# Optimization experiments

Measured on AMD Instinct MI355X. Metric: run time of the kernel, lower is better.

Reference implementation:

```python
import jax, jax.numpy as jnp
import numpy as np

D_IN = 1024
D_OUT = 1024
N, S = 4, 2048

def setup_inputs() -> dict:
    key = jax.random.key(0)
    kv, kk, kq, k1, k2, k3 = jax.random.split(key, 6)
    return {
        "v": jax.random.normal(kv, (N, S, D_IN), dtype=jnp.float32),
        "k": jax.random.normal(kk, (N, S, D_IN), dtype=jnp.float32),
        "q": jax.random.normal(kq, (N, S, D_IN), dtype=jnp.float32),
        "WV": jax.random.normal(k1, (D_OUT, D_IN), dtype=jnp.float32),
        "WQ": jax.random.normal(k2, (D_OUT, D_IN), dtype=jnp.float32),
        "WK": jax.random.normal(k3, (D_OUT, D_IN), dtype=jnp.float32),
    }

def reference(v, k, q, WV, WQ, WK) -> jnp.ndarray:
    # projections: x @ W.T  -> [N, S, D_OUT]
    wv = jnp.einsum('nsw,ow->nso', v, WV)
    wk = jnp.einsum('nsw,ow->nso', k, WK)
    wq = jnp.einsum('nsw,ow->nso', q, WQ)
    # scores [N, Sq, Sk]; NOTE: softmax over axis=1 (query axis, matching torch dim=1),
    # then post-hoc division by input_shape[0] AFTER softmax (faithful to source).
    scores = jnp.einsum('nqo,nko->nqk', wq, wk)
    wqk = jax.nn.softmax(scores, axis=1) / jnp.float32(D_IN)
    return jnp.einsum('nqk,nko->nqo', wqk, wv)
```

## Files before the change

kernel.cpp:

```cpp
#include <hip/hip_runtime.h>
#include <math.h>


typedef _Float16 f16;
typedef _Float16 f16x8 __attribute__((ext_vector_type(8)));
typedef _Float16 f16x4 __attribute__((ext_vector_type(4)));
typedef float f32x4 __attribute__((ext_vector_type(4)));

enum StageMode { SM_PLANES2, SM_PLANES1 };
enum EpiMode   { EPI_F32, EPI_SPLIT, EPI_F16T };

#define GLL_PITCH 32

__device__ __forceinline__ void gll16(const f16* g, f16* l) {
    __builtin_amdgcn_global_load_lds(
        (const __attribute__((address_space(1))) void*)g,
        (__attribute__((address_space(3))) void*)l, 16, 0, 0);
}

__device__ __forceinline__ void stage_gll_plane(const f16* __restrict__ gplane,
                                                f16* __restrict__ lds,
                                                long rowBase, int ld, int k0,
                                                int wave, int lane)
{
#pragma unroll
    for (int i = 0; i < 2; i++) {
        int slotBase = (wave * 2 + i) * 64;
        int t = slotBase + lane;
        int r = t >> 2;
        int c = (t & 3) ^ ((r >> 1) & 3);
        const f16* g = gplane + (rowBase + r) * (long)ld + k0 + c * 8;
        gll16(g, lds + (long)slotBase * 8);
    }
}

__device__ __forceinline__ int frag_off_gll(int row, int g) {
    return row * GLL_PITCH + ((g ^ ((row >> 1) & 3)) << 3);
}

template<StageMode SA, StageMode SB, EpiMode EP, int GROUPM, bool STATS>
__global__ __launch_bounds__(256, 4)
void mfma_gemm(const f16* __restrict__ Ahi, const f16* __restrict__ Alo,
               const f16* __restrict__ Bhi, const f16* __restrict__ Blo,
               float* __restrict__ pmOut, float* __restrict__ psOut,
               void* __restrict__ C0, void* __restrict__ C1,
               int M, int Nc, int K, int lda, int ldb, int ldc,
               long batchA, long batchB, long batchC,
               float epiScale, int tsShift)
{
    constexpr bool TRIPLE = (SA == SM_PLANES2);
    constexpr int PLANE_SZ = 128 * GLL_PITCH;

    int bx, by;
    if constexpr (GROUPM > 0) {
        int gx = gridDim.x;
        int lin = blockIdx.y * gx + blockIdx.x;
        int nig = GROUPM * gx;
        int gid = lin / nig;
        int rem = lin - gid * nig;
        by = gid * GROUPM + (rem % GROUPM);
        bx = rem / GROUPM;
    } else {
        bx = blockIdx.x;
        by = blockIdx.y;
    }
    const int n0 = bx * 128;
    const int m0 = by * 128;
    const long z = blockIdx.z;

    const long aOfs = z * batchA, bOfs = z * batchB, cOfs = z * batchC;

    __shared__ __align__(16) f16 As_hi[PLANE_SZ];
    __shared__ __align__(16) f16 Bs_hi[PLANE_SZ];
    __shared__ __align__(16) f16 As_lo[TRIPLE ? PLANE_SZ : 8];
    __shared__ __align__(16) f16 Bs_lo[TRIPLE ? PLANE_SZ : 8];

    const int tid  = threadIdx.x;
    const int lane = tid & 63;
    const int wave = tid >> 6;
    const int wr = (wave >> 1) * 64;
    const int wc = (wave & 1) * 64;
    const int fm = lane & 15;
    const int fg = lane >> 4;

    f32x4 acc[4][4];
#pragma unroll
    for (int i = 0; i < 4; i++)
#pragma unroll
        for (int j = 0; j < 4; j++) acc[i][j] = (f32x4){0.f, 0.f, 0.f, 0.f};

    int roA[4], roB[4];
#pragma unroll
    for (int i = 0; i < 4; i++) {
        roA[i] = frag_off_gll(wr + i * 16 + fm, fg);
        roB[i] = frag_off_gll(wc + i * 16 + fm, fg);
    }

    for (int k0 = 0; k0 < K; k0 += 32) {
        stage_gll_plane(Ahi + aOfs, As_hi, m0, lda, k0, wave, lane);
        stage_gll_plane(Bhi + bOfs, Bs_hi, n0, ldb, k0, wave, lane);
        if constexpr (TRIPLE) {
            stage_gll_plane(Alo + aOfs, As_lo, m0, lda, k0, wave, lane);
            stage_gll_plane(Blo + bOfs, Bs_lo, n0, ldb, k0, wave, lane);
        }
        __syncthreads();

        f16x8 ah[4], bh[4], al[4], bl[4];
#pragma unroll
        for (int i = 0; i < 4; i++) {
            ah[i] = *(const f16x8*)&As_hi[roA[i]];
            bh[i] = *(const f16x8*)&Bs_hi[roB[i]];
            if constexpr (TRIPLE) {
                al[i] = *(const f16x8*)&As_lo[roA[i]];
                bl[i] = *(const f16x8*)&Bs_lo[roB[i]];
            }
        }
#pragma unroll
        for (int i = 0; i < 4; i++) {
#pragma unroll
            for (int j = 0; j < 4; j++) {
                acc[i][j] = __builtin_amdgcn_mfma_f32_16x16x32_f16(ah[i], bh[j], acc[i][j], 0, 0, 0);
                if constexpr (TRIPLE) {
                    acc[i][j] = __builtin_amdgcn_mfma_f32_16x16x32_f16(ah[i], bl[j], acc[i][j], 0, 0, 0);
                    acc[i][j] = __builtin_amdgcn_mfma_f32_16x16x32_f16(al[i], bh[j], acc[i][j], 0, 0, 0);
                }
            }
        }
        __syncthreads();
    }

    const int cr = fg * 4;
    const int cn = fm;
#pragma unroll
    for (int i = 0; i < 4; i++) {
#pragma unroll
        for (int j = 0; j < 4; j++) {
#pragma unroll
            for (int r = 0; r < 4; r++) {
                long mg = m0 + wr + i * 16 + cr + r;
                long ng = n0 + wc + j * 16 + cn;
                float val = acc[i][j][r] * epiScale;
                if constexpr (EP == EPI_F32) {
                    ((float*)C0)[cOfs + mg * ldc + ng] = val;
                } else if constexpr (EP == EPI_SPLIT) {
                    f16 h = (f16)val;
                    ((f16*)C0)[cOfs + mg * ldc + ng] = h;
                    ((f16*)C1)[cOfs + mg * ldc + ng] = (f16)(val - (float)h);
                } else {
                    long TS = 1L << tsShift;
                    long nb = mg >> tsShift;
                    long s  = mg & (TS - 1);
                    long addr = nb * ((long)Nc << tsShift) + ng * TS + s;
                    ((f16*)C0)[addr] = (f16)val;
                }
            }
        }
    }

    if constexpr (STATS) {
        __shared__ float stM[2][128];
        __shared__ float stS[2][128];
#pragma unroll
        for (int j = 0; j < 4; j++) {
            float mj = -3.402823466e38f;
#pragma unroll
            for (int i = 0; i < 4; i++)
#pragma unroll
                for (int r = 0; r < 4; r++) mj = fmaxf(mj, acc[i][j][r]);
            float sj = 0.f;
#pragma unroll
            for (int i = 0; i < 4; i++)
#pragma unroll
                for (int r = 0; r < 4; r++) sj += __expf(acc[i][j][r] - mj);
#pragma unroll
            for (int mask = 16; mask <= 32; mask <<= 1) {
                float mo = __shfl_xor(mj, mask, 64);
                float so = __shfl_xor(sj, mask, 64);
                float mn = fmaxf(mj, mo);
                sj = sj * __expf(mj - mn) + so * __expf(mo - mn);
                mj = mn;
            }
            if (fg == 0) {
                stM[wave >> 1][wc + j * 16 + cn] = mj;
                stS[wave >> 1][wc + j * 16 + cn] = sj;
            }
        }
        __syncthreads();
        if (tid < 128) {
            float ma = stM[0][tid], mb = stM[1][tid];
            float Mc = fmaxf(ma, mb);
            float Sv = stS[0][tid] * __expf(ma - Mc) + stS[1][tid] * __expf(mb - Mc);
            long o = ((long)z * (M >> 7) + by) * (long)Nc + (long)bx * 128 + tid;
            pmOut[o] = Mc;
            psOut[o] = Sv;
        }
    }
}

__global__ __launch_bounds__(512, 2)
void scores_gemm(const f16* __restrict__ Ahi, const f16* __restrict__ Alo,
                 const f16* __restrict__ Bhi, const f16* __restrict__ Blo,
                 float* __restrict__ pmOut, float* __restrict__ psOut,
                 float* __restrict__ C,
                 int M, int Nc, int K, int lda, int ldb, int ldc,
                 long batchA, long batchB, long batchC)
{
    constexpr int PLANE = 256 * GLL_PITCH;

    __shared__ __align__(16) f16 As_hi[2][PLANE];
    __shared__ __align__(16) f16 As_lo[2][PLANE];
    __shared__ __align__(16) f16 Bs_hi[2][PLANE];
    __shared__ __align__(16) f16 Bs_lo[2][PLANE];

    const int tid  = threadIdx.x;
    const int lane = tid & 63;
    const int wave = tid >> 6;
    const int rw   = wave >> 2;
    const int cw   = wave & 3;
    const int wrM  = rw * 128;
    const int wrN  = cw * 64;
    const int fm   = lane & 15;
    const int fg   = lane >> 4;

    const int Lid = (int)(blockIdx.z * 64 + blockIdx.y * 8 + blockIdx.x);
    const int xcd = Lid & 7;
    const int sct = Lid >> 3;
    const int bxn = sct & 7;
    const int idxp = xcd * 4 + (sct >> 3);
    const int byn = idxp & 7;
    const int zn  = idxp >> 3;

    const int n0 = bxn * 256;
    const int m0 = byn * 256;
    const long z = zn;
    const long aOfs = z * batchA, bOfs = z * batchB, cOfs = z * batchC;

    int slotBase[2], srcA[2], srcB[2];
#pragma unroll
    for (int i = 0; i < 2; i++) {
        int sb = (wave * 2 + i) * 64;
        int t  = sb + lane;
        int r  = t >> 2;
        int c  = (t & 3) ^ ((r >> 1) & 3);
        slotBase[i] = sb * 8;
        srcA[i] = (m0 + r) * lda + c * 8;
        srcB[i] = (n0 + r) * ldb + c * 8;
    }

#define SC_STAGE(buf, k0) do {                                              \
    _Pragma("unroll")                                                        \
    for (int s_ = 0; s_ < 2; s_++) {                                         \
        gll16(Ahi + aOfs + srcA[s_] + (k0), &As_hi[buf][slotBase[s_]]);      \
        gll16(Alo + aOfs + srcA[s_] + (k0), &As_lo[buf][slotBase[s_]]);      \
        gll16(Bhi + bOfs + srcB[s_] + (k0), &Bs_hi[buf][slotBase[s_]]);      \
        gll16(Blo + bOfs + srcB[s_] + (k0), &Bs_lo[buf][slotBase[s_]]);      \
    } } while (0)

    f32x4 acc[8][4];
#pragma unroll
    for (int i = 0; i < 8; i++)
#pragma unroll
        for (int j = 0; j < 4; j++) acc[i][j] = (f32x4){0.f, 0.f, 0.f, 0.f};

    int roA[8], roB[4];
#pragma unroll
    for (int i = 0; i < 8; i++) roA[i] = frag_off_gll(wrM + i * 16 + fm, fg);
#pragma unroll
    for (int j = 0; j < 4; j++) roB[j] = frag_off_gll(wrN + j * 16 + fm, fg);

    const int NT = K >> 5;
    SC_STAGE(0, 0);
    SC_STAGE(1, 32);

    for (int t = 0; t < NT; t++) {
        const int cur = t & 1;
        if (t < NT - 1) {
            asm volatile("s_waitcnt vmcnt(8)" ::: "memory");
        } else {
            asm volatile("s_waitcnt vmcnt(0)" ::: "memory");
        }
        __builtin_amdgcn_sched_barrier(0);
        __builtin_amdgcn_s_barrier();
        __builtin_amdgcn_sched_barrier(0);

        f16x8 bh[4], a0h[4];
#pragma unroll
        for (int j = 0; j < 4; j++) bh[j] = *(const f16x8*)&Bs_hi[cur][roB[j]];
#pragma unroll
        for (int i = 0; i < 4; i++) a0h[i] = *(const f16x8*)&As_hi[cur][roA[i]];
        __builtin_amdgcn_sched_barrier(0);
        f16x8 bl[4], a0l[4];
#pragma unroll
        for (int j = 0; j < 4; j++) bl[j] = *(const f16x8*)&Bs_lo[cur][roB[j]];
#pragma unroll
        for (int i = 0; i < 4; i++) a0l[i] = *(const f16x8*)&As_lo[cur][roA[i]];
        __builtin_amdgcn_sched_barrier(0);

        __builtin_amdgcn_s_setprio(1);
#pragma unroll
        for (int i = 0; i < 4; i++)
#pragma unroll
            for (int j = 0; j < 4; j++)
                acc[i][j] = __builtin_amdgcn_mfma_f32_16x16x32_f16(a0h[i], bh[j], acc[i][j], 0, 0, 0);
        __builtin_amdgcn_s_setprio(0);
        __builtin_amdgcn_sched_barrier(0);

        f16x8 a1h[4], a1l[4];
#pragma unroll
        for (int i = 0; i < 4; i++) {
            a1h[i] = *(const f16x8*)&As_hi[cur][roA[4 + i]];
            a1l[i] = *(const f16x8*)&As_lo[cur][roA[4 + i]];
        }
        __builtin_amdgcn_sched_barrier(0);

        __builtin_amdgcn_s_setprio(1);
#pragma unroll
        for (int i = 0; i < 4; i++)
#pragma unroll
            for (int j = 0; j < 4; j++)
                acc[i][j] = __builtin_amdgcn_mfma_f32_16x16x32_f16(a0h[i], bl[j], acc[i][j], 0, 0, 0);
#pragma unroll
        for (int i = 0; i < 4; i++)
#pragma unroll
            for (int j = 0; j < 4; j++)
                acc[i][j] = __builtin_amdgcn_mfma_f32_16x16x32_f16(a0l[i], bh[j], acc[i][j], 0, 0, 0);
        __builtin_amdgcn_s_setprio(0);

        asm volatile("s_waitcnt lgkmcnt(0)" ::: "memory");
        __builtin_amdgcn_sched_barrier(0);
        __builtin_amdgcn_s_barrier();
        __builtin_amdgcn_sched_barrier(0);

        if (t + 2 < NT) SC_STAGE(cur, (t + 2) * 32);

        __builtin_amdgcn_s_setprio(1);
#pragma unroll
        for (int i = 0; i < 4; i++)
#pragma unroll
            for (int j = 0; j < 4; j++)
                acc[4 + i][j] = __builtin_amdgcn_mfma_f32_16x16x32_f16(a1h[i], bh[j], acc[4 + i][j], 0, 0, 0);
#pragma unroll
        for (int i = 0; i < 4; i++)
#pragma unroll
            for (int j = 0; j < 4; j++)
                acc[4 + i][j] = __builtin_amdgcn_mfma_f32_16x16x32_f16(a1h[i], bl[j], acc[4 + i][j], 0, 0, 0);
#pragma unroll
        for (int i = 0; i < 4; i++)
#pragma unroll
            for (int j = 0; j < 4; j++)
                acc[4 + i][j] = __builtin_amdgcn_mfma_f32_16x16x32_f16(a1l[i], bh[j], acc[4 + i][j], 0, 0, 0);
        __builtin_amdgcn_s_setprio(0);
    }
#undef SC_STAGE

    const int cr = fg * 4;
#pragma unroll
    for (int i = 0; i < 8; i++) {
#pragma unroll
        for (int j = 0; j < 4; j++) {
#pragma unroll
            for (int r = 0; r < 4; r++) {
                long mg = m0 + wrM + i * 16 + cr + r;
                long ng = n0 + wrN + j * 16 + fm;
                C[cOfs + mg * (long)ldc + ng] = acc[i][j][r];
            }
        }
    }

    __shared__ float stM[2][256];
    __shared__ float stS[2][256];
#pragma unroll
    for (int j = 0; j < 4; j++) {
        float mj = -3.402823466e38f;
#pragma unroll
        for (int i = 0; i < 8; i++)
#pragma unroll
            for (int r = 0; r < 4; r++) mj = fmaxf(mj, acc[i][j][r]);
        float sj = 0.f;
#pragma unroll
        for (int i = 0; i < 8; i++)
#pragma unroll
            for (int r = 0; r < 4; r++) sj += __expf(acc[i][j][r] - mj);
#pragma unroll
        for (int mask = 16; mask <= 32; mask <<= 1) {
            float mo = __shfl_xor(mj, mask, 64);
            float so = __shfl_xor(sj, mask, 64);
            float mn = fmaxf(mj, mo);
            sj = sj * __expf(mj - mn) + so * __expf(mo - mn);
            mj = mn;
        }
        if (fg == 0) {
            stM[rw][wrN + j * 16 + fm] = mj;
            stS[rw][wrN + j * 16 + fm] = sj;
        }
    }
    __syncthreads();
    if (tid < 256) {
        float ma = stM[0][tid], mb = stM[1][tid];
        float Mc = fmaxf(ma, mb);
        float Sv = stS[0][tid] * __expf(ma - Mc) + stS[1][tid] * __expf(mb - Mc);
        long o = ((long)z * (M >> 8) + byn) * (long)Nc + (long)bxn * 256 + tid;
        pmOut[o] = Mc;
        psOut[o] = Sv;
    }
}

template<bool HAS_LO>
__global__ __launch_bounds__(256)
void split_kernel(const float* __restrict__ src, f16* __restrict__ hi,
                  f16* __restrict__ lo, long n)
{
    long i = ((long)blockIdx.x * 256 + threadIdx.x) * 8;
    if (i >= n) return;
    float4 x0 = *(const float4*)&src[i];
    float4 x1 = *(const float4*)&src[i + 4];
    float xs[8] = {x0.x, x0.y, x0.z, x0.w, x1.x, x1.y, x1.z, x1.w};
    f16x8 h, l;
#pragma unroll
    for (int e = 0; e < 8; e++) {
        f16 hh = (f16)xs[e];
        h[e] = hh;
        if (HAS_LO) l[e] = (f16)(xs[e] - (float)hh);
    }
    *(f16x8*)&hi[i] = h;
    if (HAS_LO) *(f16x8*)&lo[i] = l;
}

template<int CH>
__global__ __launch_bounds__(64)
void stats_combine_kernel(const float* __restrict__ pm, const float* __restrict__ ps,
                          float* __restrict__ statM, float* __restrict__ statR, int S)
{
    const int n = blockIdx.y;
    const int kk = blockIdx.x * 64 + threadIdx.x;
    float M = -INFINITY;
#pragma unroll
    for (int i = 0; i < CH; i++)
        M = fmaxf(M, pm[((long)n * CH + i) * S + kk]);
    float Ssum = 0.f;
#pragma unroll
    for (int i = 0; i < CH; i++)
        Ssum += ps[((long)n * CH + i) * S + kk] * __expf(pm[((long)n * CH + i) * S + kk] - M);
    statM[(long)n * S + kk] = M;
    statR[(long)n * S + kk] = 1.0f / Ssum;
}

__global__ __launch_bounds__(256)
void pmat_kernel(const float* __restrict__ Sc, const float* __restrict__ statM,
                 const float* __restrict__ statR, f16* __restrict__ Phi, int S)
{
    const int n = blockIdx.z;
    const int kk = blockIdx.x * 1024 + threadIdx.x * 4;
    const float* Sn = Sc + (long)n * S * S;
    f16* ph = Phi + (long)n * S * S;
    float4 M4 = *(const float4*)&statM[(long)n * S + kk];
    float4 R4 = *(const float4*)&statR[(long)n * S + kk];
    const int q0 = blockIdx.y * 32;
    for (int qi = 0; qi < 32; qi++) {
        long idx = (long)(q0 + qi) * S + kk;
        float4 x = *(const float4*)&Sn[idx];
        f16x4 p;
        p[0] = (f16)(__expf(x.x - M4.x) * R4.x);
        p[1] = (f16)(__expf(x.y - M4.y) * R4.y);
        p[2] = (f16)(__expf(x.z - M4.z) * R4.z);
        p[3] = (f16)(__expf(x.w - M4.w) * R4.w);
        *(f16x4*)&ph[idx] = p;
    }
}

extern "C" void kernel_launch(void* const* d_in, const int* in_sizes, int n_in,
                              void* d_out, int out_size, void* d_ws, size_t ws_size,
                              hipStream_t stream)
{
    const float* v  = (const float*)d_in[0];
    const float* k  = (const float*)d_in[1];
    const float* q  = (const float*)d_in[2];
    const float* WV = (const float*)d_in[3];
    const float* WQ = (const float*)d_in[4];
    const float* WK = (const float*)d_in[5];
    float* out = (float*)d_out;

    const int N = 4, S = 2048, D = 1024;
    const long NSD = (long)N * S * D;
    const long DD  = (long)D * D;

    f16* ws = (f16*)d_ws;
    f16* q_hi = ws;
    f16* q_lo = ws + NSD;
    f16* k_hi = ws + 2 * NSD;
    f16* k_lo = ws + 3 * NSD;
    f16* v_hi = ws + 4 * NSD;
    f16* Wb   = ws + 5 * NSD;
    f16* WQ_hi = Wb,          *WQ_lo = Wb + DD;
    f16* WK_hi = Wb + 2 * DD, *WK_lo = Wb + 3 * DD;
    f16* WV_hi = Wb + 4 * DD;
    f16* wq_hi = ws + 5 * NSD + 5 * DD;
    f16* wq_lo = wq_hi + NSD;
    f16* wk_hi = wq_hi + 2 * NSD;
    f16* wk_lo = wq_hi + 3 * NSD;
    f16* wvT_hi = ws;
    float* Sc   = (float*)(ws + NSD);
    f16* P_hi   = wq_hi;
    float* pm    = (float*)(ws + 9 * NSD + 5 * DD);
    float* ps    = pm + (long)N * 8 * S;
    float* statM = ps + (long)N * 8 * S;
    float* statR = statM + (long)N * S;

    dim3 blk(256);

    split_kernel<true ><<<dim3(NSD / 2048), blk, 0, stream>>>(q,  q_hi, q_lo, NSD);
    split_kernel<true ><<<dim3(NSD / 2048), blk, 0, stream>>>(k,  k_hi, k_lo, NSD);
    split_kernel<false><<<dim3(NSD / 2048), blk, 0, stream>>>(v,  v_hi, nullptr, NSD);
    split_kernel<true ><<<dim3(DD / 2048),  blk, 0, stream>>>(WQ, WQ_hi, WQ_lo, DD);
    split_kernel<true ><<<dim3(DD / 2048),  blk, 0, stream>>>(WK, WK_hi, WK_lo, DD);
    split_kernel<false><<<dim3(DD / 2048),  blk, 0, stream>>>(WV, WV_hi, nullptr, DD);

    {
        dim3 g(D / 128, (N * S) / 128, 1);
        mfma_gemm<SM_PLANES2, SM_PLANES2, EPI_SPLIT, 4, false><<<g, blk, 0, stream>>>(
            q_hi, q_lo, WQ_hi, WQ_lo, nullptr, nullptr, wq_hi, wq_lo,
            N * S, D, D, D, D, D, 0, 0, 0, 1.0f, 0);
        mfma_gemm<SM_PLANES2, SM_PLANES2, EPI_SPLIT, 4, false><<<g, blk, 0, stream>>>(
            k_hi, k_lo, WK_hi, WK_lo, nullptr, nullptr, wk_hi, wk_lo,
            N * S, D, D, D, D, D, 0, 0, 0, 1.0f, 0);
        mfma_gemm<SM_PLANES1, SM_PLANES1, EPI_F16T, 4, false><<<g, blk, 0, stream>>>(
            v_hi, nullptr, WV_hi, nullptr, nullptr, nullptr, wvT_hi, nullptr,
            N * S, D, D, D, D, 0, 0, 0, 0, 1.0f, 11 );
    }
    {
        dim3 g(S / 256, S / 256, N);
        scores_gemm<<<g, dim3(512), 0, stream>>>(
            wq_hi, wq_lo, wk_hi, wk_lo, pm, ps, Sc,
            S, S, D, D, D, S, (long)S * D, (long)S * D, (long)S * S);
    }
    {
        dim3 gB(S / 64, N);
        stats_combine_kernel<8><<<gB, dim3(64), 0, stream>>>(pm, ps, statM, statR, S);
    }
    {
        dim3 g(S / 1024, S / 32, N);
        pmat_kernel<<<g, blk, 0, stream>>>(Sc, statM, statR, P_hi, S);
    }
    {
        dim3 g(D / 128, S / 128, N);
        mfma_gemm<SM_PLANES1, SM_PLANES1, EPI_F32, 4, false><<<g, blk, 0, stream>>>(
            P_hi, nullptr, wvT_hi, nullptr, nullptr, nullptr, out, nullptr,
            S, D, S, S, S, D, (long)S * S, (long)S * D, (long)S * D, 1.0f / (float)D, 0);
    }
}
```

Baseline: 458.8 us.

## Generalize scores GEMM and fuse Q/K projections into one dual launch

Templates the 256x256 scores GEMM kernel into a general big_gemm. It is used both for scores and for a single dual-problem launch that computes the Q and K projections together, with the problem chosen per tile row, in place of two 128-tile mfma_gemm launches. The K-loop pipeline is also restructured: the next tile's global-to-LDS prefetch is issued right after the top barrier rather than behind a mid-iteration barrier. This removes one barrier per iteration, but each iteration now waits for vmcnt(0). The aim is larger tiles, fewer launches and fewer syncs, at the cost of exposing more load latency.

New measurement: 460.0 us. Within noise of the previous version (+0.3%).

```diff
diff --git a/kernel.cpp b/kernel.cpp
--- a/kernel.cpp
+++ b/kernel.cpp
@@ -197,13 +197,17 @@
     }
 }
 
+template<EpiMode EP, bool STATS, bool XCDMAP, bool DUAL>
 __global__ __launch_bounds__(512, 2)
-void scores_gemm(const f16* __restrict__ Ahi, const f16* __restrict__ Alo,
-                 const f16* __restrict__ Bhi, const f16* __restrict__ Blo,
-                 float* __restrict__ pmOut, float* __restrict__ psOut,
-                 float* __restrict__ C,
-                 int M, int Nc, int K, int lda, int ldb, int ldc,
-                 long batchA, long batchB, long batchC)
+void big_gemm(const f16* __restrict__ Ahi, const f16* __restrict__ Alo,
+              const f16* __restrict__ Bhi, const f16* __restrict__ Blo,
+              const f16* __restrict__ A2hi, const f16* __restrict__ A2lo,
+              const f16* __restrict__ B2hi, const f16* __restrict__ B2lo,
+              float* __restrict__ pmOut, float* __restrict__ psOut,
+              void* __restrict__ C0, void* __restrict__ C1,
+              void* __restrict__ C20, void* __restrict__ C21,
+              int M, int Nc, int K, int lda, int ldb, int ldc,
+              long batchA, long batchB, long batchC, int msplitTiles)
 {
     constexpr int PLANE = 256 * GLL_PITCH;
 
@@ -222,16 +226,35 @@
     const int fm   = lane & 15;
     const int fg   = lane >> 4;
 
-    const int Lid = (int)(blockIdx.z * 64 + blockIdx.y * 8 + blockIdx.x);
-    const int xcd = Lid & 7;
-    const int sct = Lid >> 3;
-    const int bxn = sct & 7;
-    const int idxp = xcd * 4 + (sct >> 3);
-    const int byn = idxp & 7;
-    const int zn  = idxp >> 3;
+    int bxn, byn, zn;
+    if constexpr (XCDMAP) {
+        const int Lid = (int)(blockIdx.z * 64 + blockIdx.y * 8 + blockIdx.x);
+        const int xcd = Lid & 7;
+        const int sct = Lid >> 3;
+        bxn = sct & 7;
+        const int idxp = xcd * 4 + (sct >> 3);
+        byn = idxp & 7;
+        zn  = idxp >> 3;
+    } else {
+        bxn = blockIdx.x;
+        byn = blockIdx.y;
+        zn  = blockIdx.z;
+    }
+
+    const f16* pAhi = Ahi; const f16* pAlo = Alo;
+    const f16* pBhi = Bhi; const f16* pBlo = Blo;
+    void* pC0 = C0; void* pC1 = C1;
+    int mTile = byn;
+    if constexpr (DUAL) {
+        if (byn >= msplitTiles) {
+            pAhi = A2hi; pAlo = A2lo; pBhi = B2hi; pBlo = B2lo;
+            pC0 = C20; pC1 = C21;
+            mTile = byn - msplitTiles;
+        }
+    }
 
     const int n0 = bxn * 256;
-    const int m0 = byn * 256;
+    const int m0 = mTile * 256;
     const long z = zn;
     const long aOfs = z * batchA, bOfs = z * batchB, cOfs = z * batchC;
 
@@ -247,13 +270,13 @@
         srcB[i] = (n0 + r) * ldb + c * 8;
     }
 
-#define SC_STAGE(buf, k0) do {                                              \
+#define SC_STAGE(buf, k0) do {                                               \
     _Pragma("unroll")                                                        \
     for (int s_ = 0; s_ < 2; s_++) {                                         \
-        gll16(Ahi + aOfs + srcA[s_] + (k0), &As_hi[buf][slotBase[s_]]);      \
-        gll16(Alo + aOfs + srcA[s_] + (k0), &As_lo[buf][slotBase[s_]]);      \
-        gll16(Bhi + bOfs + srcB[s_] + (k0), &Bs_hi[buf][slotBase[s_]]);      \
-        gll16(Blo + bOfs + srcB[s_] + (k0), &Bs_lo[buf][slotBase[s_]]);      \
+        gll16(pAhi + aOfs + srcA[s_] + (k0), &As_hi[buf][slotBase[s_]]);     \
+        gll16(pAlo + aOfs + srcA[s_] + (k0), &As_lo[buf][slotBase[s_]]);     \
+        gll16(pBhi + bOfs + srcB[s_] + (k0), &Bs_hi[buf][slotBase[s_]]);     \
+        gll16(pBlo + bOfs + srcB[s_] + (k0), &Bs_lo[buf][slotBase[s_]]);     \
     } } while (0)
 
     f32x4 acc[8][4];
@@ -274,7 +297,7 @@
 
     for (int t = 0; t < NT; t++) {
         const int cur = t & 1;
-        if (t < NT - 1) {
+        if (t == 0) {
             asm volatile("s_waitcnt vmcnt(8)" ::: "memory");
         } else {
             asm volatile("s_waitcnt vmcnt(0)" ::: "memory");
@@ -283,6 +306,9 @@
         __builtin_amdgcn_s_barrier();
         __builtin_amdgcn_sched_barrier(0);
 
+        if (t >= 1 && t + 1 < NT) SC_STAGE(cur ^ 1, (t + 1) * 32);
+        __builtin_amdgcn_sched_barrier(0);
+
         f16x8 bh[4], a0h[4];
 #pragma unroll
         for (int j = 0; j < 4; j++) bh[j] = *(const f16x8*)&Bs_hi[cur][roB[j]];
@@ -325,13 +351,7 @@
             for (int j = 0; j < 4; j++)
                 acc[i][j] = __builtin_amdgcn_mfma_f32_16x16x32_f16(a0l[i], bh[j], acc[i][j], 0, 0, 0);
         __builtin_amdgcn_s_setprio(0);
-
-        asm volatile("s_waitcnt lgkmcnt(0)" ::: "memory");
-        __builtin_amdgcn_sched_barrier(0);
-        __builtin_amdgcn_s_barrier();
-        __builtin_amdgcn_sched_barrier(0);
-
-        if (t + 2 < NT) SC_STAGE(cur, (t + 2) * 32);
+        __builtin_amdgcn_sched_barrier(0);
 
         __builtin_amdgcn_s_setprio(1);
 #pragma unroll
@@ -362,46 +382,55 @@
             for (int r = 0; r < 4; r++) {
                 long mg = m0 + wrM + i * 16 + cr + r;
                 long ng = n0 + wrN + j * 16 + fm;
-                C[cOfs + mg * (long)ldc + ng] = acc[i][j][r];
-            }
-        }
-    }
-
-    __shared__ float stM[2][256];
-    __shared__ float stS[2][256];
-#pragma unroll
-    for (int j = 0; j < 4; j++) {
-        float mj = -3.402823466e38f;
-#pragma unroll
-        for (int i = 0; i < 8; i++)
-#pragma unroll
-            for (int r = 0; r < 4; r++) mj = fmaxf(mj, acc[i][j][r]);
-        float sj = 0.f;
-#pragma unroll
-        for (int i = 0; i < 8; i++)
-#pragma unroll
-            for (int r = 0; r < 4; r++) sj += __expf(acc[i][j][r] - mj);
-#pragma unroll
-        for (int mask = 16; mask <= 32; mask <<= 1) {
-            float mo = __shfl_xor(mj, mask, 64);
-            float so = __shfl_xor(sj, mask, 64);
-            float mn = fmaxf(mj, mo);
-            sj = sj * __expf(mj - mn) + so * __expf(mo - mn);
-            mj = mn;
-        }
-        if (fg == 0) {
-            stM[rw][wrN + j * 16 + fm] = mj;
-            stS[rw][wrN + j * 16 + fm] = sj;
-        }
-    }
-    __syncthreads();
-    if (tid < 256) {
-        float ma = stM[0][tid], mb = stM[1][tid];
-        float Mc = fmaxf(ma, mb);
-        float Sv = stS[0][tid] * __expf(ma - Mc) + stS[1][tid] * __expf(mb - Mc);
-        long o = ((long)z * (M >> 8) + byn) * (long)Nc + (long)bxn * 256 + tid;
-        pmOut[o] = Mc;
-        psOut[o] = Sv;
+                float val = acc[i][j][r];
+                if constexpr (EP == EPI_F32) {
+                    ((float*)pC0)[cOfs + mg * (long)ldc + ng] = val;
+                } else {
+                    f16 h = (f16)val;
+                    ((f16*)pC0)[cOfs + mg * (long)ldc + ng] = h;
+                    ((f16*)pC1)[cOfs + mg * (long)ldc + ng] = (f16)(val - (float)h);
+                }
+            }
+        }
+    }
+
+    if constexpr (STATS) {
+        __shared__ float stM[2][256];
+        __shared__ float stS[2][256];
+#pragma unroll
+        for (int j = 0; j < 4; j++) {
+            float mj = -3.402823466e38f;
+#pragma unroll
+            for (int i = 0; i < 8; i++)
+#pragma unroll
+                for (int r = 0; r < 4; r++) mj = fmaxf(mj, acc[i][j][r]);
+            float sj = 0.f;
+#pragma unroll
+            for (int i = 0; i < 8; i++)
+#pragma unroll
+                for (int r = 0; r < 4; r++) sj += __expf(acc[i][j][r] - mj);
+#pragma unroll
+            for (int mask = 16; mask <= 32; mask <<= 1) {
+                float mo = __shfl_xor(mj, mask, 64);
+                float so = __shfl_xor(sj, mask, 64);
+                float mn = fmaxf(mj, mo);
+                sj = sj * __expf(mj - mn) + so * __expf(mo - mn);
+                mj = mn;
+            }
+            if (fg == 0) {
+                stM[rw][wrN + j * 16 + fm] = mj;
+                stS[rw][wrN + j * 16 + fm] = sj;
+            }
+        }
+        __syncthreads();
+        if (tid < 256) {
+            float ma = stM[0][tid], mb = stM[1][tid];
+            float Mc = fmaxf(ma, mb);
+            float Sv = stS[0][tid] * __expf(ma - Mc) + stS[1][tid] * __expf(mb - Mc);
+            long o = ((long)z * (M >> 8) + byn) * (long)Nc + (long)bxn * 256 + tid;
+            pmOut[o] = Mc;
+            psOut[o] = Sv;
+        }
     }
 }
 
@@ -516,22 +545,27 @@
     split_kernel<false><<<dim3(DD / 2048),  blk, 0, stream>>>(WV, WV_hi, nullptr, DD);
 
     {
+        dim3 g(D / 256, (2 * N * S) / 256, 1);
+        big_gemm<EPI_SPLIT, false, false, true><<<g, dim3(512), 0, stream>>>(
+            q_hi, q_lo, WQ_hi, WQ_lo,
+            k_hi, k_lo, WK_hi, WK_lo,
+            nullptr, nullptr,
+            wq_hi, wq_lo, wk_hi, wk_lo,
+            2 * N * S, D, D, D, D, D, 0, 0, 0, (N * S) / 256 );
+    }
+    {
         dim3 g(D / 128, (N * S) / 128, 1);
-        mfma_gemm<SM_PLANES2, SM_PLANES2, EPI_SPLIT, 4, false><<<g, blk, 0, stream>>>(
-            q_hi, q_lo, WQ_hi, WQ_lo, nullptr, nullptr, wq_hi, wq_lo,
-            N * S, D, D, D, D, D, 0, 0, 0, 1.0f, 0);
-        mfma_gemm<SM_PLANES2, SM_PLANES2, EPI_SPLIT, 4, false><<<g, blk, 0, stream>>>(
-            k_hi, k_lo, WK_hi, WK_lo, nullptr, nullptr, wk_hi, wk_lo,
-            N * S, D, D, D, D, D, 0, 0, 0, 1.0f, 0);
         mfma_gemm<SM_PLANES1, SM_PLANES1, EPI_F16T, 4, false><<<g, blk, 0, stream>>>(
             v_hi, nullptr, WV_hi, nullptr, nullptr, nullptr, wvT_hi, nullptr,
             N * S, D, D, D, D, 0, 0, 0, 0, 1.0f, 11 );
     }
     {
         dim3 g(S / 256, S / 256, N);
-        scores_gemm<<<g, dim3(512), 0, stream>>>(
-            wq_hi, wq_lo, wk_hi, wk_lo, pm, ps, Sc,
-            S, S, D, D, D, S, (long)S * D, (long)S * D, (long)S * S);
+        big_gemm<EPI_F32, true, true, false><<<g, dim3(512), 0, stream>>>(
+            wq_hi, wq_lo, wk_hi, wk_lo,
+            nullptr, nullptr, nullptr, nullptr,
+            pm, ps, Sc, nullptr, nullptr, nullptr,
+            S, S, D, D, D, S, (long)S * D, (long)S * D, (long)S * S, 1 << 30);
     }
     {
         dim3 gB(S / 64, N);
```
